# Kernel tuning notes

Hardware: AMD Instinct MI355X
Metric: run time of the kernel (lower is better)

The kernel has to match this reference:

```python
import jax, jax.numpy as jnp
import numpy as np

# The 8 structuring elements from the torch module, in order.
_KERNELS = np.array([
    [[1.,1.,1.],[1.,1.,1.],[1.,1.,1.]],
    [[0.,1.,1.],[0.,1.,1.],[0.,1.,1.]],
    [[1.,1.,1.],[1.,1.,1.],[0.,0.,0.]],
    [[0.,0.,0.],[0.,1.,1.],[0.,1.,1.]],
    [[0.,1.,0.],[0.,1.,0.],[0.,1.,0.]],
    [[0.,0.,0.],[1.,1.,1.],[0.,0.,0.]],
    [[0.,1.,0.],[0.,1.,0.],[0.,0.,0.]],
    [[0.,0.,0.],[1.,1.,0.],[0.,0.,0.]],
], dtype=np.float32)


def _conv3x3(x, k):
    # x: [N,1,H,W], k: [3,3] -> same-padded single-channel conv (cross-correlation, like torch conv2d)
    return jax.lax.conv_general_dilated(
        x, k[None, None, :, :], window_strides=(1, 1),
        padding=((1, 1), (1, 1)),
        dimension_numbers=('NCHW', 'OIHW', 'NCHW'))


def setup_inputs() -> dict:
    key = jax.random.key(0)
    N, H, W = 16, 1024, 1024
    x = (jax.random.uniform(key, (N, 1, H, W)) < 0.5).astype(jnp.float32)
    kernels = jnp.asarray(_KERNELS)  # [8,3,3]
    return {"x": x, "kernels": kernels}


def reference(x, kernels):
    output = jnp.zeros_like(x)
    # Sequential loop over the 8 fixed structuring elements (data dependency on x).
    for i in range(8):
        k = kernels[i]
        eroded = _conv3x3(x, k)
        ksum = jnp.sum(k)
        mask = (eroded >= ksum).astype(x.dtype)
        output = jnp.maximum(output, mask)
        # mark(): dilate the mask with the flipped binarized kernel
        dil_k = jnp.flip((k > 0).astype(x.dtype), axis=(0, 1))
        visited = (_conv3x3(mask, dil_k) > 0).astype(x.dtype)
        x = x - visited
    # return_single_point=True branch
    sp = _conv3x3(output, kernels[0])
    output = jnp.where((sp > 0) & (sp < 2), jnp.ones_like(sp), jnp.zeros_like(sp))
    return output
```

## Files before the change

### kernel.cpp

```cpp
#include <hip/hip_runtime.h>
#include <stdint.h>


typedef unsigned long long u64;

#define WIDTH   1024
#define HEIGHT  1024
#define NIMG    16
#define WPR     16
#define TH      64
#define PR      98
#define PW      18
#define NTHR    512

__global__ __launch_bounds__(256) void pack_kernel(const float* __restrict__ x,
                                                   u64* __restrict__ packed) {
    int rowg = blockIdx.x;
    int tid  = threadIdx.x;
    int wv   = tid >> 6;
    int lane = tid & 63;
    const float* base = x + (size_t)rowg * WIDTH + wv * 256;
    u64* pbase = packed + (size_t)rowg * WPR + wv * 4;
    #pragma unroll
    for (int j = 0; j < 4; ++j) {
        float f = base[j * 64 + lane];
        u64 m = __ballot(f > 0.5f);
        if (lane == 0) pbase[j] = m;
    }
}

template <int CM>
__device__ __forceinline__ u64 hand(const u64* Ar, int w) {
    u64 c = Ar[w], res = ~0ULL;
    if (CM & 2) res &= c;
    if (CM & 1) res &= (c << 1) | (Ar[w - 1] >> 63);
    if (CM & 4) res &= (c >> 1) | (Ar[w + 1] << 63);
    return res;
}
template <int CM>
__device__ __forceinline__ u64 hor(const u64* Ar, int w) {
    u64 c = Ar[w], res = 0;
    if (CM & 2) res |= c;
    if (CM & 1) res |= (c >> 1) | (Ar[w + 1] << 63);
    if (CM & 4) res |= (c << 1) | (Ar[w - 1] >> 63);
    return res;
}
template <int RM>
__device__ __forceinline__ u64 vand(const u64 (*A)[PW], int r, int w) {
    u64 res = ~0ULL;
    if (RM & 1) res &= A[r - 1][w];
    if (RM & 2) res &= A[r][w];
    if (RM & 4) res &= A[r + 1][w];
    return res;
}
template <int RM>
__device__ __forceinline__ u64 vor(const u64 (*A)[PW], int r, int w) {
    u64 res = 0;
    if (RM & 1) res |= A[r + 1][w];
    if (RM & 2) res |= A[r][w];
    if (RM & 4) res |= A[r - 1][w];
    return res;
}

template <int R, typename F>
__device__ __forceinline__ void forcells(F f) {
    for (int idx = threadIdx.x; idx < (TH + 2 * R) * WPR; idx += NTHR) {
        int r = 17 - R + (idx >> 4);
        int w = 1 + (idx & 15);
        f(r, w);
    }
    __syncthreads();
}

template <int RM, int CM, int HR, int MR, int DHR, int BR, bool DIL>
__device__ __forceinline__ void morph_step(u64 (&B)[PR][PW], u64 (&T)[PR][PW],
                                           u64 (&M)[PR][PW], u64 (&O)[PR][PW]) {
    if (CM != 2 && RM != 2) {
        forcells<HR>([&](int r, int w) { T[r][w] = hand<CM>(B[r], w); });
        forcells<MR>([&](int r, int w) {
            u64 m = vand<RM>(T, r, w); M[r][w] = m; O[r][w] |= m;
        });
    } else if (CM == 2) {
        forcells<MR>([&](int r, int w) {
            u64 m = vand<RM>(B, r, w); M[r][w] = m; O[r][w] |= m;
        });
    } else {
        forcells<MR>([&](int r, int w) {
            u64 m = hand<CM>(B[r], w); M[r][w] = m; O[r][w] |= m;
        });
    }
    if (DIL) {
        if (CM != 2 && RM != 2) {
            forcells<DHR>([&](int r, int w) { T[r][w] = hor<CM>(M[r], w); });
            forcells<BR>([&](int r, int w) { B[r][w] &= ~vor<RM>(T, r, w); });
        } else if (CM == 2) {
            forcells<BR>([&](int r, int w) { B[r][w] &= ~vor<RM>(M, r, w); });
        } else {
            forcells<BR>([&](int r, int w) { B[r][w] &= ~hor<CM>(M[r], w); });
        }
    }
}

__global__ __launch_bounds__(NTHR) void morph_kernel(const u64* __restrict__ packed,
                                                     float* __restrict__ out) {
    __shared__ u64 B[PR][PW];
    __shared__ u64 T[PR][PW];
    __shared__ u64 M[PR][PW];
    __shared__ u64 O[PR][PW];
    int tid = threadIdx.x;
    int ty = blockIdx.x, img = blockIdx.y;

    {
        u64* bf = &B[0][0]; u64* mf = &M[0][0]; u64* of = &O[0][0];
        for (int i = tid; i < PR * PW; i += NTHR) { bf[i] = 0; mf[i] = 0; of[i] = 0; }
    }
    __syncthreads();

    const u64* pimg = packed + (size_t)img * HEIGHT * WPR;
    for (int idx = tid; idx < (TH + 32) * WPR; idx += NTHR) {
        int rr = idx >> 4, w = idx & 15;
        int gy = ty * TH - 16 + rr;
        if (gy >= 0 && gy < HEIGHT)
            B[rr + 1][w + 1] = pimg[(size_t)gy * WPR + w];
    }
    __syncthreads();

    morph_step<7, 7, 16, 15, 15, 14, true >(B, T, M, O);
    morph_step<7, 6, 14, 13, 13, 12, true >(B, T, M, O);
    morph_step<3, 7, 12, 11, 11, 10, true >(B, T, M, O);
    morph_step<6, 6, 10,  9,  9,  8, true >(B, T, M, O);
    morph_step<7, 2,  8,  7,  7,  6, true >(B, T, M, O);
    morph_step<2, 7,  6,  5,  5,  4, true >(B, T, M, O);
    morph_step<3, 2,  4,  3,  3,  2, true >(B, T, M, O);
    morph_step<2, 3,  2,  1,  1,  0, false>(B, T, M, O);

    forcells<0>([&](int r, int w) {
        u64 ones = 0;
        u64 twos = 0;
        #pragma unroll
        for (int dr = -1; dr <= 1; ++dr) {
            const u64* Ar = O[r + dr];
            u64 c  = Ar[w];
            u64 wv = (c << 1) | (Ar[w - 1] >> 63);
            u64 ev = (c >> 1) | (Ar[w + 1] << 63);
            twos |= ones & wv; ones ^= wv;
            twos |= ones & c;  ones ^= c;
            twos |= ones & ev; ones ^= ev;
        }
        T[r][w] = ones & ~twos;
    });

    float* obase = out + ((size_t)img * HEIGHT + (size_t)ty * TH) * WIDTH;
    for (int idx = tid; idx < TH * (WIDTH / 4); idx += NTHR) {
        int row = idx >> 8;
        int q   = idx & 255;
        u64 word = T[17 + row][1 + (q >> 4)];
        int b = (q & 15) * 4;
        float4 v;
        v.x = (float)((word >> (b + 0)) & 1ULL);
        v.y = (float)((word >> (b + 1)) & 1ULL);
        v.z = (float)((word >> (b + 2)) & 1ULL);
        v.w = (float)((word >> (b + 3)) & 1ULL);
        *(float4*)(obase + (size_t)row * WIDTH + q * 4) = v;
    }
}

extern "C" void kernel_launch(void* const* d_in, const int* in_sizes, int n_in,
                              void* d_out, int out_size, void* d_ws, size_t ws_size,
                              hipStream_t stream) {
    const float* x = (const float*)d_in[0];
    float* out = (float*)d_out;
    u64* packed = (u64*)d_ws;

    hipLaunchKernelGGL(pack_kernel, dim3(NIMG * HEIGHT), dim3(256), 0, stream, x, packed);
    hipLaunchKernelGGL(morph_kernel, dim3(HEIGHT / TH, NIMG), dim3(NTHR), 0, stream,
                       packed, out);
}
```

Measured before the change: 125.9 us.

## Fuse bit-packing into morphology kernel with smaller tiles and nontemporal stores

Drops the separate pack kernel and the packed workspace round trip. Each block now reads float rows directly and packs them to bitmasks with ballot inside the morphology kernel. Tile height shrinks from 64 to 32 rows (256 threads) to give more blocks, so the 16-row halo, which is re-read from float input, is a larger fraction of each tile. Output writes switch to nontemporal stores.

```diff
diff --git a/kernel.cpp b/kernel.cpp
--- a/kernel.cpp
+++ b/kernel.cpp
@@ -3,31 +3,18 @@
 
 
 typedef unsigned long long u64;
+typedef float vfloat4 __attribute__((ext_vector_type(4)));
 
 #define WIDTH   1024
 #define HEIGHT  1024
 #define NIMG    16
 #define WPR     16
-#define TH      64
-#define PR      98
+#define TH      32
+#define HALO    16
+#define RR      (TH + 2 * HALO)
+#define PR      (RR + 2)
 #define PW      18
-#define NTHR    512
-
-__global__ __launch_bounds__(256) void pack_kernel(const float* __restrict__ x,
-                                                   u64* __restrict__ packed) {
-    int rowg = blockIdx.x;
-    int tid  = threadIdx.x;
-    int wv   = tid >> 6;
-    int lane = tid & 63;
-    const float* base = x + (size_t)rowg * WIDTH + wv * 256;
-    u64* pbase = packed + (size_t)rowg * WPR + wv * 4;
-    #pragma unroll
-    for (int j = 0; j < 4; ++j) {
-        float f = base[j * 64 + lane];
-        u64 m = __ballot(f > 0.5f);
-        if (lane == 0) pbase[j] = m;
-    }
-}
+#define NTHR    256
 
 template <int CM>
 __device__ __forceinline__ u64 hand(const u64* Ar, int w) {
@@ -101,8 +88,8 @@
     }
 }
 
-__global__ __launch_bounds__(NTHR) void morph_kernel(const u64* __restrict__ packed,
-                                                     float* __restrict__ out) {
+__global__ __launch_bounds__(NTHR) void skel_kernel(const float* __restrict__ x,
+                                                    float* __restrict__ out) {
     __shared__ u64 B[PR][PW];
     __shared__ u64 T[PR][PW];
     __shared__ u64 M[PR][PW];
@@ -116,12 +103,21 @@
     }
     __syncthreads();
 
-    const u64* pimg = packed + (size_t)img * HEIGHT * WPR;
-    for (int idx = tid; idx < (TH + 32) * WPR; idx += NTHR) {
-        int rr = idx >> 4, w = idx & 15;
-        int gy = ty * TH - 16 + rr;
-        if (gy >= 0 && gy < HEIGHT)
-            B[rr + 1][w + 1] = pimg[(size_t)gy * WPR + w];
+    {
+        int wv = tid >> 6, lane = tid & 63;
+        const float* ximg = x + (size_t)img * HEIGHT * WIDTH;
+        for (int rr = wv; rr < RR; rr += NTHR / 64) {
+            int gy = ty * TH - HALO + rr;
+            if (gy >= 0 && gy < HEIGHT) {
+                const float* rbase = ximg + (size_t)gy * WIDTH + lane;
+                #pragma unroll
+                for (int w16 = 0; w16 < 16; ++w16) {
+                    float f = rbase[w16 * 64];
+                    u64 m = __ballot(f > 0.5f);
+                    if (lane == 0) B[rr + 1][w16 + 1] = m;
+                }
+            }
+        }
     }
     __syncthreads();
 
@@ -156,12 +152,12 @@
         int q   = idx & 255;
         u64 word = T[17 + row][1 + (q >> 4)];
         int b = (q & 15) * 4;
-        float4 v;
+        vfloat4 v;
         v.x = (float)((word >> (b + 0)) & 1ULL);
         v.y = (float)((word >> (b + 1)) & 1ULL);
         v.z = (float)((word >> (b + 2)) & 1ULL);
         v.w = (float)((word >> (b + 3)) & 1ULL);
-        *(float4*)(obase + (size_t)row * WIDTH + q * 4) = v;
+        __builtin_nontemporal_store(v, (vfloat4*)(obase + (size_t)row * WIDTH + q * 4));
     }
 }
 
@@ -170,9 +166,6 @@
                               hipStream_t stream) {
     const float* x = (const float*)d_in[0];
     float* out = (float*)d_out;
-    u64* packed = (u64*)d_ws;
-
-    hipLaunchKernelGGL(pack_kernel, dim3(NIMG * HEIGHT), dim3(256), 0, stream, x, packed);
-    hipLaunchKernelGGL(morph_kernel, dim3(HEIGHT / TH, NIMG), dim3(NTHR), 0, stream,
-                       packed, out);
+    hipLaunchKernelGGL(skel_kernel, dim3(HEIGHT / TH, NIMG), dim3(NTHR), 0, stream,
+                       x, out);
 }
```

New measurement: 185.6 us. 47.4% more time.
